# Performance work log

Measured on AMD Instinct MI355X. Metric: run time of the kernel, lower is better.

## Reference

```python
import jax, jax.numpy as jnp
import numpy as np

N_NODES = 50000
N_EDGES = 800000


def _sage_mean(x, src, dst, w, W_self, W_neigh, b, n_nodes):
    # DGL SAGEConv('mean') with edge_weight: messages m_e = w_e * h[src_e],
    # h_neigh[v] = sum_{e->v} m_e / in_degree(v)  (zero if no in-edges),
    # out = h @ W_self + h_neigh @ W_neigh + b
    msg = x[src] * w[:, None]                                   # [E, d]
    s = jax.ops.segment_sum(msg, dst, num_segments=n_nodes)     # [N, d]
    deg = jax.ops.segment_sum(jnp.ones_like(w), dst, num_segments=n_nodes)
    h_neigh = s / jnp.clip(deg, 1.0)[:, None]
    return x @ W_self + h_neigh @ W_neigh + b


def setup_inputs() -> dict:
    key = jax.random.key(0)
    ks = jax.random.split(key, 12)
    d_in, d_h = 64, 256
    inp = {
        'features': jax.random.normal(ks[0], (N_NODES, d_in), dtype=jnp.float32),
        'edge_src': jax.random.randint(ks[1], (N_EDGES,), 0, N_NODES, dtype=jnp.int32),
        'edge_dst': jax.random.randint(ks[2], (N_EDGES,), 0, N_NODES, dtype=jnp.int32),
        'edge_weights': jax.random.uniform(ks[3], (N_EDGES,), dtype=jnp.float32),
        'W1_self': jax.random.normal(ks[4], (d_in, d_h), dtype=jnp.float32) * (1.0 / np.sqrt(d_in)),
        'W1_neigh': jax.random.normal(ks[5], (d_in, d_h), dtype=jnp.float32) * (1.0 / np.sqrt(d_in)),
        'b1': jnp.zeros((d_h,), dtype=jnp.float32),
        'W2_self': jax.random.normal(ks[6], (d_h, 128), dtype=jnp.float32) * (1.0 / np.sqrt(d_h)),
        'W2_neigh': jax.random.normal(ks[7], (d_h, 128), dtype=jnp.float32) * (1.0 / np.sqrt(d_h)),
        'b2': jnp.zeros((128,), dtype=jnp.float32),
        'Wl1': jax.random.normal(ks[8], (128, 64), dtype=jnp.float32) * (1.0 / np.sqrt(128)),
        'bl1': jnp.zeros((64,), dtype=jnp.float32),
        'Wl2': jax.random.normal(ks[9], (64, 32), dtype=jnp.float32) * (1.0 / np.sqrt(64)),
        'bl2': jnp.zeros((32,), dtype=jnp.float32),
        'Wl3': jax.random.normal(ks[10], (32, 10), dtype=jnp.float32) * (1.0 / np.sqrt(32)),
        'bl3': jnp.zeros((10,), dtype=jnp.float32),
    }
    return inp


def reference(features, edge_src, edge_dst, edge_weights,
              W1_self, W1_neigh, b1, W2_self, W2_neigh, b2,
              Wl1, bl1, Wl2, bl2, Wl3, bl3):
    n = features.shape[0]
    x = features.reshape(n, -1)  # flatten (already 2D)
    x = jax.nn.relu(_sage_mean(x, edge_src, edge_dst, edge_weights,
                               W1_self, W1_neigh, b1, n))
    # conv2 is applied twice on identical inputs in the original; results are equal
    embeddings = _sage_mean(x, edge_src, edge_dst, edge_weights,
                            W2_self, W2_neigh, b2, n)
    h = jax.nn.relu(embeddings @ Wl1 + bl1)
    h = jax.nn.relu(h @ Wl2 + bl2)
    out = h @ Wl3 + bl3
    return (out, embeddings)
```

## Files before the change

### kernel.cpp

```cpp
#include <hip/hip_runtime.h>
#include <hip/hip_bf16.h>

#define N_NODES 50000
#define N_EDGES 800000
#define MT_TILES 3125

#define NBLK_SORT 400
#define CHUNK_SORT 2000
#define NBKT 196

typedef __attribute__((ext_vector_type(8))) short frag_ab;
typedef __attribute__((ext_vector_type(4))) float frag_cd;

static __device__ __forceinline__ unsigned short f2b(float f) {
    union { float f; unsigned u; } v; v.f = f;
    unsigned r = v.u + 0x7fffu + ((v.u >> 16) & 1u);
    return (unsigned short)(r >> 16);
}
static __device__ __forceinline__ float b2f(unsigned short b) {
    union { float f; unsigned u; } v; v.u = ((unsigned)b) << 16;
    return v.f;
}
static __device__ __forceinline__ float blo(unsigned p) { return b2f((unsigned short)(p & 0xffffu)); }
static __device__ __forceinline__ float bhi(unsigned p) { return b2f((unsigned short)(p >> 16)); }

static __device__ __forceinline__ unsigned short packBK_elem(const float* __restrict__ Wa,
                                                             const float* __restrict__ Wb,
                                                             int Ka, int N, int idx) {
    int j = idx & 7;
    int lane = (idx >> 3) & 63;
    int rest = idx >> 9;
    int ntiles = N >> 4;
    int nt = rest % ntiles;
    int kt = rest / ntiles;
    int kk = kt * 32 + (lane >> 4) * 8 + j;
    int nn = nt * 16 + (lane & 15);
    float v = (kk < Ka) ? Wa[kk * N + nn] : Wb[(kk - Ka) * N + nn];
    return f2b(v);
}
static __device__ __forceinline__ unsigned short packBN_elem(const float* __restrict__ Wa,
                                                             const float* __restrict__ Wb,
                                                             int Na, int N, int idx) {
    int j = idx & 7;
    int lane = (idx >> 3) & 63;
    int rest = idx >> 9;
    int ntiles = N >> 4;
    int nt = rest % ntiles;
    int kt = rest / ntiles;
    int kk = kt * 32 + (lane >> 4) * 8 + j;
    int nn = nt * 16 + (lane & 15);
    float v = (nn < Na) ? Wa[kk * Na + nn] : Wb[kk * (N - Na) + (nn - Na)];
    return f2b(v);
}

#define PREP_S0 800000
#define PREP_S1 (PREP_S0 + 32768)
#define PREP_S2 (PREP_S1 + 65536)
#define PREP_S3 (PREP_S2 + 8192)
#define PREP_S4 (PREP_S3 + 2048)
#define PREP_BLKS 3549

__global__ __launch_bounds__(256) void prep_p1_kernel(const float4* __restrict__ x4,
                                                      ushort4* __restrict__ xb4,
                                                      const float* __restrict__ W1s,
                                                      const float* __restrict__ W1n,
                                                      const float* __restrict__ W2s,
                                                      const float* __restrict__ W2n,
                                                      const float* __restrict__ Wl1,
                                                      const float* __restrict__ Wl2,
                                                      unsigned short* __restrict__ B1p,
                                                      unsigned short* __restrict__ B2p,
                                                      unsigned short* __restrict__ Bl1p,
                                                      unsigned short* __restrict__ Bl2p,
                                                      const int* __restrict__ dst,
                                                      int* __restrict__ G) {
    __shared__ int h[256];
    int bid = blockIdx.x;
    int t = threadIdx.x;
    if (bid >= PREP_BLKS) {
        int blk = bid - PREP_BLKS;
        h[t] = 0;
        __syncthreads();
        int base = blk * CHUNK_SORT;
        for (int i = t; i < CHUNK_SORT; i += 256)
            atomicAdd(&h[dst[base + i] >> 8], 1);
        __syncthreads();
        G[blk * 256 + t] = h[t];
        return;
    }
    int idx = bid * 256 + t;
    if (idx < PREP_S0) {
        float4 v = x4[idx];
        ushort4 o;
        o.x = f2b(v.x); o.y = f2b(v.y); o.z = f2b(v.z); o.w = f2b(v.w);
        xb4[idx] = o;
    } else if (idx < PREP_S1) {
        int i = idx - PREP_S0;
        B1p[i] = packBK_elem(W1s, W1n, 64, 256, i);
    } else if (idx < PREP_S2) {
        int i = idx - PREP_S1;
        B2p[i] = packBN_elem(W2s, W2n, 128, 256, i);
    } else if (idx < PREP_S3) {
        int i = idx - PREP_S2;
        Bl1p[i] = packBK_elem(Wl1, Wl1, 128, 64, i);
    } else {
        int i = idx - PREP_S3;
        Bl2p[i] = packBK_elem(Wl2, Wl2, 64, 32, i);
    }
}


__global__ __launch_bounds__(256) void p2a_scan(int* __restrict__ G,
                                                int* __restrict__ colsum) {
    __shared__ int sc[256];
    int b = blockIdx.x;
    int t = threadIdx.x;
    int j0 = 2 * t, j1 = 2 * t + 1;
    int v0 = (j0 < NBLK_SORT) ? G[j0 * 256 + b] : 0;
    int v1 = (j1 < NBLK_SORT) ? G[j1 * 256 + b] : 0;
    int v = v0 + v1;
    sc[t] = v;
    __syncthreads();
    for (int off = 1; off < 256; off <<= 1) {
        int add = (t >= off) ? sc[t - off] : 0;
        __syncthreads();
        sc[t] += add;
        __syncthreads();
    }
    int ex = sc[t] - v;
    if (j0 < NBLK_SORT) G[j0 * 256 + b] = ex;
    if (j1 < NBLK_SORT) G[j1 * 256 + b] = ex + v0;
    if (t == 255) colsum[b] = sc[255];
}

__global__ __launch_bounds__(256) void p3_scatter(const int* __restrict__ src,
                                                  const int* __restrict__ dst,
                                                  const float* __restrict__ w,
                                                  const int* __restrict__ G,
                                                  const int* __restrict__ colsum,
                                                  int* __restrict__ bdst,
                                                  int2* __restrict__ bsedge) {
    __shared__ int cur[256];
    __shared__ int sc[256];
    int t = threadIdx.x;
    int v = colsum[t];
    sc[t] = v;
    __syncthreads();
    for (int off = 1; off < 256; off <<= 1) {
        int add = (t >= off) ? sc[t - off] : 0;
        __syncthreads();
        sc[t] += add;
        __syncthreads();
    }
    cur[t] = G[blockIdx.x * 256 + t] + (sc[t] - v);
    __syncthreads();
    int base = blockIdx.x * CHUNK_SORT;
    for (int i = t; i < CHUNK_SORT; i += 256) {
        int e = base + i;
        int d = dst[e];
        int pos = atomicAdd(&cur[d >> 8], 1);
        bdst[pos] = d;
        bsedge[pos] = make_int2(src[e], __float_as_int(w[e]));
    }
}

__global__ __launch_bounds__(256) void p4_sort(const int* __restrict__ colsum,
                                               const int* __restrict__ bdst,
                                               const int2* __restrict__ bsedge,
                                               int* __restrict__ row_off,
                                               float* __restrict__ inv_deg,
                                               int2* __restrict__ sedge) {
    __shared__ int lcnt[256];
    __shared__ int lcur[256];
    __shared__ int sc[256];
    __shared__ int sE0, sE1;
    int t = threadIdx.x;
    int b = blockIdx.x;
    int cv = colsum[t];
    sc[t] = cv;
    __syncthreads();
    for (int off = 1; off < 256; off <<= 1) {
        int add = (t >= off) ? sc[t - off] : 0;
        __syncthreads();
        sc[t] += add;
        __syncthreads();
    }
    if (t == b) { sE0 = sc[t] - cv; sE1 = sc[t]; }
    lcnt[t] = 0;
    __syncthreads();
    int e0 = sE0, e1 = sE1;
    int d0 = b << 8;
    for (int e = e0 + t; e < e1; e += 256)
        atomicAdd(&lcnt[bdst[e] - d0], 1);
    __syncthreads();
    int v = lcnt[t];
    sc[t] = v;
    __syncthreads();
    for (int off = 1; off < 256; off <<= 1) {
        int add = (t >= off) ? sc[t - off] : 0;
        __syncthreads();
        sc[t] += add;
        __syncthreads();
    }
    int loff = e0 + sc[t] - v;
    lcur[t] = loff;
    int d = d0 + t;
    if (d < N_NODES) {
        row_off[d] = loff;
        inv_deg[d] = 1.0f / (float)(v > 0 ? v : 1);
    }
    if (b == 0 && t == 0) row_off[N_NODES] = N_EDGES;
    __syncthreads();
    for (int e = e0 + t; e < e1; e += 256) {
        int dd = bdst[e];
        int2 sv = bsedge[e];
        int pos = atomicAdd(&lcur[dd - d0], 1);
        sedge[pos] = sv;
    }
}


__global__ __launch_bounds__(256) void agg64_kernel(const uint4* __restrict__ xb4,
                                                    const int* __restrict__ row_off,
                                                    const int2* __restrict__ sedge,
                                                    const float* __restrict__ inv_deg,
                                                    uint4* __restrict__ hn1b4) {
    int tid = threadIdx.x;
    int lane = tid & 63;
    int er = lane >> 3;
    int l7 = lane & 7;
    int n = blockIdx.x * 4 + (tid >> 6);
    if (n >= N_NODES) return;
    int e0 = row_off[n], e1 = row_off[n + 1];
    float id = inv_deg[n];
    float a[8];
    #pragma unroll
    for (int j = 0; j < 8; j++) a[j] = 0.f;
    int e1m1 = e1 - 1;
    for (int e = e0; e < e1; e += 16) {
        int2 m[2];
        uint4 p[2];
        float w[2];
        #pragma unroll
        for (int k = 0; k < 2; k++) {
            int ee = e + k * 8 + er;
            int idx = ee < e1 ? ee : e1m1;
            m[k] = sedge[idx];
        }
        #pragma unroll
        for (int k = 0; k < 2; k++) {
            p[k] = xb4[m[k].x * 8 + l7];
            int ee = e + k * 8 + er;
            w[k] = (ee < e1) ? __int_as_float(m[k].y) : 0.f;
        }
        #pragma unroll
        for (int k = 0; k < 2; k++) {
            a[0] += w[k] * blo(p[k].x); a[1] += w[k] * bhi(p[k].x);
            a[2] += w[k] * blo(p[k].y); a[3] += w[k] * bhi(p[k].y);
            a[4] += w[k] * blo(p[k].z); a[5] += w[k] * bhi(p[k].z);
            a[6] += w[k] * blo(p[k].w); a[7] += w[k] * bhi(p[k].w);
        }
    }
    #pragma unroll
    for (int j = 0; j < 8; j++) {
        a[j] += __shfl_xor(a[j], 8, 64);
        a[j] += __shfl_xor(a[j], 16, 64);
        a[j] += __shfl_xor(a[j], 32, 64);
    }
    if (er == 0) {
        uint4 o;
        o.x = (unsigned)f2b(a[0] * id) | ((unsigned)f2b(a[1] * id) << 16);
        o.y = (unsigned)f2b(a[2] * id) | ((unsigned)f2b(a[3] * id) << 16);
        o.z = (unsigned)f2b(a[4] * id) | ((unsigned)f2b(a[5] * id) << 16);
        o.w = (unsigned)f2b(a[6] * id) | ((unsigned)f2b(a[7] * id) << 16);
        hn1b4[n * 8 + l7] = o;
    }
}

__global__ __launch_bounds__(256) void agg128_kernel(const uint4* __restrict__ zb4,
                                                     const int* __restrict__ row_off,
                                                     const int2* __restrict__ sedge,
                                                     const float* __restrict__ inv_deg,
                                                     float* __restrict__ emb) {
    int tid = threadIdx.x;
    int lane = tid & 63;
    int qr = lane >> 4;
    int l15 = lane & 15;
    int n = blockIdx.x * 4 + (tid >> 6);
    if (n >= N_NODES) return;
    int e0 = row_off[n], e1 = row_off[n + 1];
    float id = inv_deg[n];
    float4 s0, s1;
    if (qr == 0) {
        s0 = ((const float4*)emb)[n * 32 + l15 * 2];
        s1 = ((const float4*)emb)[n * 32 + l15 * 2 + 1];
    }
    float a[8];
    #pragma unroll
    for (int j = 0; j < 8; j++) a[j] = 0.f;
    int e1m1 = e1 - 1;
    for (int e = e0; e < e1; e += 16) {
        int2 m[4];
        uint4 p[4];
        float w[4];
        #pragma unroll
        for (int k = 0; k < 4; k++) {
            int ee = e + k * 4 + qr;
            int idx = ee < e1 ? ee : e1m1;
            m[k] = sedge[idx];
        }
        #pragma unroll
        for (int k = 0; k < 4; k++) {
            p[k] = zb4[m[k].x * 16 + l15];
            int ee = e + k * 4 + qr;
            w[k] = (ee < e1) ? __int_as_float(m[k].y) : 0.f;
        }
        #pragma unroll
        for (int k = 0; k < 4; k++) {
            a[0] += w[k] * blo(p[k].x); a[1] += w[k] * bhi(p[k].x);
            a[2] += w[k] * blo(p[k].y); a[3] += w[k] * bhi(p[k].y);
            a[4] += w[k] * blo(p[k].z); a[5] += w[k] * bhi(p[k].z);
            a[6] += w[k] * blo(p[k].w); a[7] += w[k] * bhi(p[k].w);
        }
    }
    #pragma unroll
    for (int j = 0; j < 8; j++) {
        a[j] += __shfl_xor(a[j], 16, 64);
        a[j] += __shfl_xor(a[j], 32, 64);
    }
    if (qr == 0) {
        float v0 = s0.x + a[0] * id;
        float v1 = s0.y + a[1] * id;
        float v2 = s0.z + a[2] * id;
        float v3 = s0.w + a[3] * id;
        float v4 = s1.x + a[4] * id;
        float v5 = s1.y + a[5] * id;
        float v6 = s1.z + a[6] * id;
        float v7 = s1.w + a[7] * id;
        ((float4*)emb)[n * 32 + l15 * 2]     = make_float4(v0, v1, v2, v3);
        ((float4*)emb)[n * 32 + l15 * 2 + 1] = make_float4(v4, v5, v6, v7);
    }
}


__global__ __launch_bounds__(512) void gemm1_mfma(const unsigned short* __restrict__ xb,
                                                  const unsigned short* __restrict__ hn1b,
                                                  const unsigned short* __restrict__ Bp,
                                                  const float* __restrict__ b1,
                                                  unsigned short* __restrict__ x1b) {
    __shared__ __align__(16) unsigned short sB[2][8192];
    int tid = threadIdx.x;
    int lane = tid & 63;
    int wv = tid >> 6;
    int mt = blockIdx.x * 8 + wv;
    if (mt >= MT_TILES) mt = MT_TILES - 1;
    int q = lane >> 4;
    int rl = lane & 15;
    int row = mt * 16 + rl;
    frag_ab a[4];
    a[0] = *(const frag_ab*)(xb + row * 64 + q * 8);
    a[1] = *(const frag_ab*)(xb + row * 64 + q * 8 + 32);
    a[2] = *(const frag_ab*)(hn1b + row * 64 + q * 8);
    a[3] = *(const frag_ab*)(hn1b + row * 64 + q * 8 + 32);
    frag_cd acc[16];
    #pragma unroll
    for (int nt = 0; nt < 16; nt++) acc[nt] = (frag_cd){0.f, 0.f, 0.f, 0.f};
    const float4* gB = (const float4*)Bp;
    float4 s0 = gB[tid], s1 = gB[512 + tid];
    ((float4*)sB[0])[tid] = s0;
    ((float4*)sB[0])[512 + tid] = s1;
    #pragma unroll
    for (int kt = 0; kt < 4; kt++) {
        __syncthreads();
        if (kt < 3) { s0 = gB[(kt + 1) * 1024 + tid]; s1 = gB[(kt + 1) * 1024 + 512 + tid]; }
        const unsigned short* sb = sB[kt & 1];
        #pragma unroll
        for (int nt = 0; nt < 16; nt++) {
            frag_ab b = *(const frag_ab*)(sb + (nt * 64 + lane) * 8);
            acc[nt] = __builtin_amdgcn_mfma_f32_16x16x32_bf16(a[kt], b, acc[nt], 0, 0, 0);
        }
        if (kt < 3) {
            ((float4*)sB[(kt + 1) & 1])[tid] = s0;
            ((float4*)sB[(kt + 1) & 1])[512 + tid] = s1;
        }
    }
    int r0 = mt * 16;
    #pragma unroll
    for (int nt = 0; nt < 16; nt++) {
        int c = nt * 16 + rl;
        float bias = b1[c];
        #pragma unroll
        for (int i = 0; i < 4; i++) {
            int r = r0 + q * 4 + i;
            float v = acc[nt][i] + bias;
            v = v > 0.f ? v : 0.f;
            x1b[r * 256 + c] = f2b(v);
        }
    }
}

__global__ __launch_bounds__(512) void gemm2_mfma(const unsigned short* __restrict__ x1b,
                                                  const unsigned short* __restrict__ Bp,
                                                  const float* __restrict__ b2,
                                                  float* __restrict__ emb,
                                                  unsigned short* __restrict__ zb) {
    __shared__ __align__(16) unsigned short sB[2][8192];
    int tid = threadIdx.x;
    int lane = tid & 63;
    int wv = tid >> 6;
    int mt = blockIdx.x * 8 + wv;
    if (mt >= MT_TILES) mt = MT_TILES - 1;
    int q = lane >> 4;
    int rl = lane & 15;
    int row = mt * 16 + rl;
    const unsigned short* arow = x1b + row * 256 + q * 8;
    frag_ab a[8];
    #pragma unroll
    for (int kt = 0; kt < 8; kt++) a[kt] = *(const frag_ab*)(arow + kt * 32);
    frag_cd acc[16];
    #pragma unroll
    for (int nt = 0; nt < 16; nt++) acc[nt] = (frag_cd){0.f, 0.f, 0.f, 0.f};
    const float4* gB = (const float4*)Bp;
    float4 s0 = gB[tid], s1 = gB[512 + tid];
    ((float4*)sB[0])[tid] = s0;
    ((float4*)sB[0])[512 + tid] = s1;
    #pragma unroll
    for (int kt = 0; kt < 8; kt++) {
        __syncthreads();
        if (kt < 7) { s0 = gB[(kt + 1) * 1024 + tid]; s1 = gB[(kt + 1) * 1024 + 512 + tid]; }
        const unsigned short* sb = sB[kt & 1];
        #pragma unroll
        for (int nt = 0; nt < 16; nt++) {
            frag_ab b = *(const frag_ab*)(sb + (nt * 64 + lane) * 8);
            acc[nt] = __builtin_amdgcn_mfma_f32_16x16x32_bf16(a[kt], b, acc[nt], 0, 0, 0);
        }
        if (kt < 7) {
            ((float4*)sB[(kt + 1) & 1])[tid] = s0;
            ((float4*)sB[(kt + 1) & 1])[512 + tid] = s1;
        }
    }
    int r0 = mt * 16;
    #pragma unroll
    for (int nt = 0; nt < 8; nt++) {
        int c = nt * 16 + rl;
        float bias = b2[c];
        #pragma unroll
        for (int i = 0; i < 4; i++) {
            int r = r0 + q * 4 + i;
            emb[r * 128 + c] = acc[nt][i] + bias;
        }
    }
    #pragma unroll
    for (int nt = 8; nt < 16; nt++) {
        int c = (nt - 8) * 16 + rl;
        #pragma unroll
        for (int i = 0; i < 4; i++) {
            int r = r0 + q * 4 + i;
            zb[r * 128 + c] = f2b(acc[nt][i]);
        }
    }
}

__global__ __launch_bounds__(256) void mlp_fused(const float* __restrict__ emb,
                                                 const unsigned short* __restrict__ B1,
                                                 const float* __restrict__ bl1,
                                                 const unsigned short* __restrict__ B2,
                                                 const float* __restrict__ bl2,
                                                 const float* __restrict__ Wl3,
                                                 const float* __restrict__ bl3,
                                                 float* __restrict__ out) {
    __shared__ __align__(16) unsigned short h64s[64 * 72];
    __shared__ float hs[64][33];
    int tid = threadIdx.x;
    int lane = tid & 63;
    int wv = tid >> 6;
    int mt = blockIdx.x * 4 + wv;
    if (mt >= MT_TILES) mt = MT_TILES - 1;
    int q = lane >> 4;
    int rl = lane & 15;
    const frag_ab* bp1 = (const frag_ab*)B1;
    frag_cd acc[4];
    #pragma unroll
    for (int nt = 0; nt < 4; nt++) acc[nt] = (frag_cd){0.f, 0.f, 0.f, 0.f};
    #pragma unroll
    for (int kt = 0; kt < 4; kt++) {
        const float4* ap = (const float4*)(emb + (mt * 16 + rl) * 128 + kt * 32 + q * 8);
        float4 f0 = ap[0], f1 = ap[1];
        frag_ab a;
        a[0] = (short)f2b(f0.x); a[1] = (short)f2b(f0.y);
        a[2] = (short)f2b(f0.z); a[3] = (short)f2b(f0.w);
        a[4] = (short)f2b(f1.x); a[5] = (short)f2b(f1.y);
        a[6] = (short)f2b(f1.z); a[7] = (short)f2b(f1.w);
        #pragma unroll
        for (int nt = 0; nt < 4; nt++)
            acc[nt] = __builtin_amdgcn_mfma_f32_16x16x32_bf16(a, bp1[(kt * 4 + nt) * 64 + lane], acc[nt], 0, 0, 0);
    }
    #pragma unroll
    for (int nt = 0; nt < 4; nt++) {
        int c = nt * 16 + rl;
        float bias = bl1[c];
        #pragma unroll
        for (int i = 0; i < 4; i++) {
            float v = acc[nt][i] + bias;
            h64s[(wv * 16 + q * 4 + i) * 72 + c] = f2b(v > 0.f ? v : 0.f);
        }
    }
    __syncthreads();
    const unsigned short* a2 = h64s + (wv * 16 + rl) * 72 + q * 8;
    const frag_ab* bp2 = (const frag_ab*)B2;
    frag_cd acc2[2];
    #pragma unroll
    for (int nt = 0; nt < 2; nt++) acc2[nt] = (frag_cd){0.f, 0.f, 0.f, 0.f};
    #pragma unroll
    for (int kt = 0; kt < 2; kt++) {
        frag_ab a = *(const frag_ab*)(a2 + kt * 32);
        #pragma unroll
        for (int nt = 0; nt < 2; nt++)
            acc2[nt] = __builtin_amdgcn_mfma_f32_16x16x32_bf16(a, bp2[(kt * 2 + nt) * 64 + lane], acc2[nt], 0, 0, 0);
    }
    #pragma unroll
    for (int nt = 0; nt < 2; nt++) {
        int c = nt * 16 + rl;
        float bias = bl2[c];
        #pragma unroll
        for (int i = 0; i < 4; i++) {
            int lr = wv * 16 + q * 4 + i;
            float v = acc2[nt][i] + bias;
            hs[lr][c] = v > 0.f ? v : 0.f;
        }
    }
    __syncthreads();
    int base = blockIdx.x * 64;
    for (int idx = tid; idx < 640; idx += 256) {
        int lr = idx / 10;
        int j = idx - lr * 10;
        int n = base + lr;
        if (n < N_NODES) {
            float a = bl3[j];
            #pragma unroll
            for (int k = 0; k < 32; k++) a += hs[lr][k] * Wl3[k * 10 + j];
            out[n * 10 + j] = a;
        }
    }
}


extern "C" void kernel_launch(void* const* d_in, const int* in_sizes, int n_in,
                              void* d_out, int out_size, void* d_ws, size_t ws_size,
                              hipStream_t stream) {
    const float* x   = (const float*)d_in[0];
    const int* esrc  = (const int*)d_in[1];
    const int* edst  = (const int*)d_in[2];
    const float* ew  = (const float*)d_in[3];
    const float* W1s = (const float*)d_in[4];
    const float* W1n = (const float*)d_in[5];
    const float* b1  = (const float*)d_in[6];
    const float* W2s = (const float*)d_in[7];
    const float* W2n = (const float*)d_in[8];
    const float* b2  = (const float*)d_in[9];
    const float* Wl1 = (const float*)d_in[10];
    const float* bl1 = (const float*)d_in[11];
    const float* Wl2 = (const float*)d_in[12];
    const float* bl2 = (const float*)d_in[13];
    const float* Wl3 = (const float*)d_in[14];
    const float* bl3 = (const float*)d_in[15];

    float* out = (float*)d_out;
    float* emb = out + 500000;

    char* ws = (char*)d_ws;
    size_t off = 0;
    auto alloc = [&](size_t bytes) -> void* {
        void* p = ws + off;
        off = (off + bytes + 255) & ~(size_t)255;
        return p;
    };
    int*   row_off = (int*)alloc((size_t)(N_NODES + 1) * 4);
    float* inv_deg = (float*)alloc((size_t)N_NODES * 4);
    int*   G       = (int*)alloc((size_t)NBLK_SORT * 256 * 4);
    int*   colsum  = (int*)alloc(256 * 4);
    int*   bdst    = (int*)alloc((size_t)N_EDGES * 4);
    int2*  bsedge  = (int2*)alloc((size_t)N_EDGES * 8);
    int2*  sedge   = (int2*)alloc((size_t)N_EDGES * 8);
    unsigned short* xb   = (unsigned short*)alloc((size_t)N_NODES * 64 * 2);
    unsigned short* hn1b = (unsigned short*)alloc((size_t)N_NODES * 64 * 2);
    unsigned short* x1b  = (unsigned short*)alloc((size_t)N_NODES * 256 * 2);
    unsigned short* zb   = (unsigned short*)alloc((size_t)N_NODES * 128 * 2);
    unsigned short* B1p  = (unsigned short*)alloc(128 * 256 * 2);
    unsigned short* B2p  = (unsigned short*)alloc(256 * 256 * 2);
    unsigned short* Bl1p = (unsigned short*)alloc(128 * 64 * 2);
    unsigned short* Bl2p = (unsigned short*)alloc(64 * 32 * 2);

    prep_p1_kernel<<<PREP_BLKS + NBLK_SORT, 256, 0, stream>>>(
        (const float4*)x, (ushort4*)xb, W1s, W1n, W2s, W2n, Wl1, Wl2,
        B1p, B2p, Bl1p, Bl2p, edst, G);

    p2a_scan<<<256, 256, 0, stream>>>(G, colsum);
    p3_scatter<<<NBLK_SORT, 256, 0, stream>>>(esrc, edst, ew, G, colsum, bdst, bsedge);
    p4_sort<<<NBKT, 256, 0, stream>>>(colsum, bdst, bsedge, row_off, inv_deg, sedge);

    const int GBLK8 = (MT_TILES + 7) / 8;
    const int GBLK  = (MT_TILES + 3) / 4;
    const int ABLK  = (N_NODES + 3) / 4;

    agg64_kernel<<<ABLK, 256, 0, stream>>>((const uint4*)xb, row_off, sedge,
                                           inv_deg, (uint4*)hn1b);
    gemm1_mfma<<<GBLK8, 512, 0, stream>>>(xb, hn1b, B1p, b1, x1b);

    gemm2_mfma<<<GBLK8, 512, 0, stream>>>(x1b, B2p, b2, emb, zb);
    agg128_kernel<<<ABLK, 256, 0, stream>>>((const uint4*)zb, row_off, sedge,
                                            inv_deg, emb);

    mlp_fused<<<GBLK, 256, 0, stream>>>(emb, Bl1p, bl1, Bl2p, bl2, Wl3, bl3, out);
}
```

Baseline: 235.0 us.

## Pack dst low bits into src field and move embedding residual add into MLP

Measured after the change: 228.4 us (median of 2 runs). -2.8%, faster.

```diff
diff --git a/kernel.cpp b/kernel.cpp
--- a/kernel.cpp
+++ b/kernel.cpp
@@ -138,7 +138,6 @@
                                                   const float* __restrict__ w,
                                                   const int* __restrict__ G,
                                                   const int* __restrict__ colsum,
-                                                  int* __restrict__ bdst,
                                                   int2* __restrict__ bsedge) {
     __shared__ int cur[256];
     __shared__ int sc[256];
@@ -159,13 +158,11 @@
         int e = base + i;
         int d = dst[e];
         int pos = atomicAdd(&cur[d >> 8], 1);
-        bdst[pos] = d;
-        bsedge[pos] = make_int2(src[e], __float_as_int(w[e]));
+        bsedge[pos] = make_int2(((d & 255) << 16) | src[e], __float_as_int(w[e]));
     }
 }
 
 __global__ __launch_bounds__(256) void p4_sort(const int* __restrict__ colsum,
-                                               const int* __restrict__ bdst,
                                                const int2* __restrict__ bsedge,
                                                int* __restrict__ row_off,
                                                float* __restrict__ inv_deg,
@@ -191,7 +188,7 @@
     int e0 = sE0, e1 = sE1;
     int d0 = b << 8;
     for (int e = e0 + t; e < e1; e += 256)
-        atomicAdd(&lcnt[bdst[e] - d0], 1);
+        atomicAdd(&lcnt[bsedge[e].x >> 16], 1);
     __syncthreads();
     int v = lcnt[t];
     sc[t] = v;
@@ -212,10 +209,10 @@
     if (b == 0 && t == 0) row_off[N_NODES] = N_EDGES;
     __syncthreads();
     for (int e = e0 + t; e < e1; e += 256) {
-        int dd = bdst[e];
-        int2 sv = bsedge[e];
-        int pos = atomicAdd(&lcur[dd - d0], 1);
-        sedge[pos] = sv;
+        int2 pk = bsedge[e];
+        int dl = pk.x >> 16;
+        int pos = atomicAdd(&lcur[dl], 1);
+        sedge[pos] = make_int2(pk.x & 0xffff, pk.y);
     }
 }
 
@@ -281,7 +278,7 @@
                                                      const int* __restrict__ row_off,
                                                      const int2* __restrict__ sedge,
                                                      const float* __restrict__ inv_deg,
-                                                     float* __restrict__ emb) {
+                                                     uint4* __restrict__ hnb4) {
     int tid = threadIdx.x;
     int lane = tid & 63;
     int qr = lane >> 4;
@@ -290,11 +287,6 @@
     if (n >= N_NODES) return;
     int e0 = row_off[n], e1 = row_off[n + 1];
     float id = inv_deg[n];
-    float4 s0, s1;
-    if (qr == 0) {
-        s0 = ((const float4*)emb)[n * 32 + l15 * 2];
-        s1 = ((const float4*)emb)[n * 32 + l15 * 2 + 1];
-    }
     float a[8];
     #pragma unroll
     for (int j = 0; j < 8; j++) a[j] = 0.f;
@@ -329,16 +321,12 @@
         a[j] += __shfl_xor(a[j], 32, 64);
     }
     if (qr == 0) {
-        float v0 = s0.x + a[0] * id;
-        float v1 = s0.y + a[1] * id;
-        float v2 = s0.z + a[2] * id;
-        float v3 = s0.w + a[3] * id;
-        float v4 = s1.x + a[4] * id;
-        float v5 = s1.y + a[5] * id;
-        float v6 = s1.z + a[6] * id;
-        float v7 = s1.w + a[7] * id;
-        ((float4*)emb)[n * 32 + l15 * 2]     = make_float4(v0, v1, v2, v3);
-        ((float4*)emb)[n * 32 + l15 * 2 + 1] = make_float4(v4, v5, v6, v7);
+        uint4 o;
+        o.x = (unsigned)f2b(a[0] * id) | ((unsigned)f2b(a[1] * id) << 16);
+        o.y = (unsigned)f2b(a[2] * id) | ((unsigned)f2b(a[3] * id) << 16);
+        o.z = (unsigned)f2b(a[4] * id) | ((unsigned)f2b(a[5] * id) << 16);
+        o.w = (unsigned)f2b(a[6] * id) | ((unsigned)f2b(a[7] * id) << 16);
+        hnb4[n * 16 + l15] = o;
     }
 }
 
@@ -402,7 +390,7 @@
 __global__ __launch_bounds__(512) void gemm2_mfma(const unsigned short* __restrict__ x1b,
                                                   const unsigned short* __restrict__ Bp,
                                                   const float* __restrict__ b2,
-                                                  float* __restrict__ emb,
+                                                  float* __restrict__ embS,
                                                   unsigned short* __restrict__ zb) {
     __shared__ __align__(16) unsigned short sB[2][8192];
     int tid = threadIdx.x;
@@ -447,7 +435,7 @@
         #pragma unroll
         for (int i = 0; i < 4; i++) {
             int r = r0 + q * 4 + i;
-            emb[r * 128 + c] = acc[nt][i] + bias;
+            embS[r * 128 + c] = acc[nt][i] + bias;
         }
     }
     #pragma unroll
@@ -461,36 +449,52 @@
     }
 }
 
-__global__ __launch_bounds__(256) void mlp_fused(const float* __restrict__ emb,
+__global__ __launch_bounds__(256) void mlp_fused(const float4* __restrict__ embS4,
+                                                 const uint2* __restrict__ hnb2,
                                                  const unsigned short* __restrict__ B1,
                                                  const float* __restrict__ bl1,
                                                  const unsigned short* __restrict__ B2,
                                                  const float* __restrict__ bl2,
                                                  const float* __restrict__ Wl3,
                                                  const float* __restrict__ bl3,
-                                                 float* __restrict__ out) {
+                                                 float* __restrict__ out,
+                                                 float4* __restrict__ emb4) {
+    __shared__ __align__(16) unsigned short embA[64 * 136];
     __shared__ __align__(16) unsigned short h64s[64 * 72];
     __shared__ float hs[64][33];
     int tid = threadIdx.x;
     int lane = tid & 63;
     int wv = tid >> 6;
+    int base_n = blockIdx.x * 64;
+    #pragma unroll
+    for (int it = 0; it < 8; it++) {
+        int idx = it * 256 + tid;
+        int r = idx >> 5;
+        int c4 = idx & 31;
+        int n = base_n + r;
+        if (n >= N_NODES) n = N_NODES - 1;
+        float4 v = embS4[(size_t)n * 32 + c4];
+        uint2 h = hnb2[(size_t)n * 32 + c4];
+        v.x += blo(h.x); v.y += bhi(h.x);
+        v.z += blo(h.y); v.w += bhi(h.y);
+        emb4[(size_t)n * 32 + c4] = v;
+        ushort4 o;
+        o.x = f2b(v.x); o.y = f2b(v.y); o.z = f2b(v.z); o.w = f2b(v.w);
+        *(ushort4*)(embA + r * 136 + c4 * 4) = o;
+    }
+    __syncthreads();
     int mt = blockIdx.x * 4 + wv;
     if (mt >= MT_TILES) mt = MT_TILES - 1;
     int q = lane >> 4;
     int rl = lane & 15;
+    const unsigned short* a1base = embA + (wv * 16 + rl) * 136 + q * 8;
     const frag_ab* bp1 = (const frag_ab*)B1;
     frag_cd acc[4];
     #pragma unroll
     for (int nt = 0; nt < 4; nt++) acc[nt] = (frag_cd){0.f, 0.f, 0.f, 0.f};
     #pragma unroll
     for (int kt = 0; kt < 4; kt++) {
-        const float4* ap = (const float4*)(emb + (mt * 16 + rl) * 128 + kt * 32 + q * 8);
-        float4 f0 = ap[0], f1 = ap[1];
-        frag_ab a;
-        a[0] = (short)f2b(f0.x); a[1] = (short)f2b(f0.y);
-        a[2] = (short)f2b(f0.z); a[3] = (short)f2b(f0.w);
-        a[4] = (short)f2b(f1.x); a[5] = (short)f2b(f1.y);
-        a[6] = (short)f2b(f1.z); a[7] = (short)f2b(f1.w);
+        frag_ab a = *(const frag_ab*)(a1base + kt * 32);
         #pragma unroll
         for (int nt = 0; nt < 4; nt++)
             acc[nt] = __builtin_amdgcn_mfma_f32_16x16x32_bf16(a, bp1[(kt * 4 + nt) * 64 + lane], acc[nt], 0, 0, 0);
@@ -530,11 +534,10 @@
         }
     }
     __syncthreads();
-    int base = blockIdx.x * 64;
     for (int idx = tid; idx < 640; idx += 256) {
         int lr = idx / 10;
         int j = idx - lr * 10;
-        int n = base + lr;
+        int n = base_n + lr;
         if (n < N_NODES) {
             float a = bl3[j];
             #pragma unroll
@@ -579,13 +582,14 @@
     float* inv_deg = (float*)alloc((size_t)N_NODES * 4);
     int*   G       = (int*)alloc((size_t)NBLK_SORT * 256 * 4);
     int*   colsum  = (int*)alloc(256 * 4);
-    int*   bdst    = (int*)alloc((size_t)N_EDGES * 4);
     int2*  bsedge  = (int2*)alloc((size_t)N_EDGES * 8);
     int2*  sedge   = (int2*)alloc((size_t)N_EDGES * 8);
     unsigned short* xb   = (unsigned short*)alloc((size_t)N_NODES * 64 * 2);
     unsigned short* hn1b = (unsigned short*)alloc((size_t)N_NODES * 64 * 2);
     unsigned short* x1b  = (unsigned short*)alloc((size_t)N_NODES * 256 * 2);
     unsigned short* zb   = (unsigned short*)alloc((size_t)N_NODES * 128 * 2);
+    unsigned short* hnb  = (unsigned short*)alloc((size_t)N_NODES * 128 * 2);
+    float* embS          = (float*)alloc((size_t)N_NODES * 128 * 4);
     unsigned short* B1p  = (unsigned short*)alloc(128 * 256 * 2);
     unsigned short* B2p  = (unsigned short*)alloc(256 * 256 * 2);
     unsigned short* Bl1p = (unsigned short*)alloc(128 * 64 * 2);
@@ -596,8 +600,8 @@
         B1p, B2p, Bl1p, Bl2p, edst, G);
 
     p2a_scan<<<256, 256, 0, stream>>>(G, colsum);
-    p3_scatter<<<NBLK_SORT, 256, 0, stream>>>(esrc, edst, ew, G, colsum, bdst, bsedge);
-    p4_sort<<<NBKT, 256, 0, stream>>>(colsum, bdst, bsedge, row_off, inv_deg, sedge);
+    p3_scatter<<<NBLK_SORT, 256, 0, stream>>>(esrc, edst, ew, G, colsum, bsedge);
+    p4_sort<<<NBKT, 256, 0, stream>>>(colsum, bsedge, row_off, inv_deg, sedge);
 
     const int GBLK8 = (MT_TILES + 7) / 8;
     const int GBLK  = (MT_TILES + 3) / 4;
@@ -607,9 +611,11 @@
                                            inv_deg, (uint4*)hn1b);
     gemm1_mfma<<<GBLK8, 512, 0, stream>>>(xb, hn1b, B1p, b1, x1b);
 
-    gemm2_mfma<<<GBLK8, 512, 0, stream>>>(x1b, B2p, b2, emb, zb);
+    gemm2_mfma<<<GBLK8, 512, 0, stream>>>(x1b, B2p, b2, embS, zb);
     agg128_kernel<<<ABLK, 256, 0, stream>>>((const uint4*)zb, row_off, sedge,
-                                            inv_deg, emb);
-
-    mlp_fused<<<GBLK, 256, 0, stream>>>(emb, Bl1p, bl1, Bl2p, bl2, Wl3, bl3, out);
-}
+                                            inv_deg, (uint4*)hnb);
+
+    mlp_fused<<<GBLK, 256, 0, stream>>>((const float4*)embS, (const uint2*)hnb,
+                                        Bl1p, bl1, Bl2p, bl2, Wl3, bl3, out,
+                                        (float4*)emb);
+}
```
